# Optimization experiments

Measured on AMD Instinct MI355X. Metric: run time of the kernel, lower is better.

Reference implementation:

```python
import jax, jax.numpy as jnp
import numpy as np

N, E, G, D, L = 200000, 400000, 1024, 300, 5
BN_EPS = 1e-5


def setup_inputs() -> dict:
    key = jax.random.key(0)
    ks = jax.random.split(key, 14)
    s = 0.1  # param init scale
    return {
        "atomic_number": jax.random.randint(ks[0], (N,), 0, 120),
        "chirality_type": jax.random.randint(ks[1], (N,), 0, 3),
        "bond_type": jax.random.randint(ks[2], (E,), 0, 6),
        "bond_direction_type": jax.random.randint(ks[3], (E,), 0, 3),
        "src": jax.random.randint(ks[4], (E,), 0, N),
        "dst": jax.random.randint(ks[5], (E,), 0, N),
        "graph_ids": jnp.sort(jax.random.randint(ks[6], (N,), 0, G)),
        "num_graphs": G,
        "node_emb0": jax.random.normal(ks[7], (120, D), jnp.float32) * s,
        "node_emb1": jax.random.normal(ks[8], (3, D), jnp.float32) * s,
        "edge_emb0": jax.random.normal(ks[9], (L, 6, D), jnp.float32) * s,
        "edge_emb1": jax.random.normal(ks[10], (L, 3, D), jnp.float32) * s,
        "W1": jax.random.normal(ks[11], (L, D, 2 * D), jnp.float32) * (1.0 / np.sqrt(D)),
        "b1": jnp.zeros((L, 2 * D), jnp.float32),
        "W2": jax.random.normal(ks[12], (L, 2 * D, D), jnp.float32) * (1.0 / np.sqrt(2 * D)),
        "b2": jnp.zeros((L, D), jnp.float32),
        "bn_gamma": jnp.ones((L, D), jnp.float32),
        "bn_beta": jnp.zeros((L, D), jnp.float32),
        "bn_mean": jnp.zeros((L, D), jnp.float32),
        "bn_var": jnp.ones((L, D), jnp.float32),
        "Wd": jax.random.normal(ks[13], (D, 256), jnp.float32) * (1.0 / np.sqrt(D)),
        "bd": jnp.zeros((256,), jnp.float32),
    }


def reference(atomic_number, chirality_type, bond_type, bond_direction_type,
              src, dst, graph_ids, num_graphs,
              node_emb0, node_emb1, edge_emb0, edge_emb1,
              W1, b1, W2, b2, bn_gamma, bn_beta, bn_mean, bn_var, Wd, bd):
    n = atomic_number.shape[0]
    # input node embedding: sum of the two categorical lookups
    h = node_emb0[atomic_number] + node_emb1[chirality_type]  # [N, D]
    for l in range(L):
        # per-layer edge embedding (sum of bond-type / bond-direction lookups)
        e = edge_emb0[l][bond_type] + edge_emb1[l][bond_direction_type]  # [E, D]
        # message u_add_e, sum reduce onto destination nodes
        m = h[src] + e
        agg = jax.ops.segment_sum(m, dst, num_segments=n)  # [N, D]
        # GIN MLP: Linear(D,2D) -> ReLU -> Linear(2D,D)
        h = jax.nn.relu(agg @ W1[l] + b1[l]) @ W2[l] + b2[l]
        # BatchNorm1d in eval mode (running stats)
        h = (h - bn_mean[l]) * jax.lax.rsqrt(bn_var[l] + BN_EPS) * bn_gamma[l] + bn_beta[l]
        if l < L - 1:  # ReLU on all but last layer (dropout is identity in eval)
            h = jax.nn.relu(h)
    # AvgPooling over nodes of each graph
    gsum = jax.ops.segment_sum(h, graph_ids, num_segments=num_graphs)  # [G, D]
    cnt = jax.ops.segment_sum(jnp.ones((n, 1), h.dtype), graph_ids, num_segments=num_graphs)
    gavg = gsum / jnp.maximum(cnt, 1.0)
    # head: Dropout (eval identity) + Linear(300, 256), then squeeze (no-op here)
    return jnp.squeeze(gavg @ Wd + bd)
```

## Files before the change

### kernel.cpp

```cpp
#include <hip/hip_runtime.h>
#include <hip/hip_bf16.h>
#include <hip/hip_fp16.h>

#define D 300
#define D2 150
#define HD 600
#define NLAYERS 5
#define BN_EPS 1e-5f

#define KS1 10
#define NT1 5
#define KS2 20
#define NT2 3
#define P1 (NT1*KS1*4096)
#define P2 (NT2*KS2*4096)

#define SCAN_BLK 1024

typedef _Float16 f16x8 __attribute__((ext_vector_type(8)));
typedef __attribute__((ext_vector_type(4))) float f32x4;

__device__ inline ushort f2h(float x) {
    __half h = __float2half(x);
    return *reinterpret_cast<ushort*>(&h);
}
__device__ inline float h2f(ushort u) {
    __half h;
    *reinterpret_cast<ushort*>(&h) = u;
    return __half2float(h);
}
__device__ inline uint pack2h(float lo, float hi) {
    return (uint)f2h(lo) | ((uint)f2h(hi) << 16);
}

__global__ __launch_bounds__(256) void zero_kernel(uint4* __restrict__ p, long n4)
{
    long i = (long)blockIdx.x * blockDim.x + threadIdx.x;
    long stride = (long)gridDim.x * blockDim.x;
    uint4 z = make_uint4(0u, 0u, 0u, 0u);
    for (; i < n4; i += stride) p[i] = z;
}

__global__ __launch_bounds__(256) void embed_kernel(
    const int* __restrict__ an, const int* __restrict__ ch,
    const float* __restrict__ e0, const float* __restrict__ e1,
    uint* __restrict__ h_u, int N)
{
    int node = blockIdx.x * 4 + (threadIdx.x >> 6);
    if (node >= N) return;
    int lane = threadIdx.x & 63;
    const float* r0 = e0 + (size_t)an[node] * D;
    const float* r1 = e1 + (size_t)ch[node] * D;
    uint* hr = h_u + (size_t)node * D2;
    for (int d2 = lane; d2 < D2; d2 += 64) {
        float2 a = *(const float2*)(r0 + d2 * 2);
        float2 b = *(const float2*)(r1 + d2 * 2);
        hr[d2] = pack2h(a.x + b.x, a.y + b.y);
    }
}

__global__ __launch_bounds__(256) void count_kernel(
    const int* __restrict__ dst, int* __restrict__ deg, int E)
{
    int e = blockIdx.x * 256 + threadIdx.x;
    if (e < E) atomicAdd(&deg[dst[e]], 1);
}

__global__ __launch_bounds__(256) void scan_part_kernel(
    const int* __restrict__ deg, int* __restrict__ part, int N)
{
    __shared__ int sm[256];
    int b = blockIdx.x, t = threadIdx.x;
    int base = b * SCAN_BLK + t * 4;
    int s = 0;
#pragma unroll
    for (int j = 0; j < 4; ++j) { int i = base + j; if (i < N) s += deg[i]; }
    sm[t] = s;
    __syncthreads();
    for (int off = 128; off > 0; off >>= 1) {
        if (t < off) sm[t] += sm[t + off];
        __syncthreads();
    }
    if (t == 0) part[b] = sm[0];
}

__global__ __launch_bounds__(256) void scan_top_kernel(int* __restrict__ part, int NB)
{
    __shared__ int sm[256];
    int t = threadIdx.x;
    int own = (t < NB) ? part[t] : 0;
    sm[t] = own;
    __syncthreads();
    for (int off = 1; off < 256; off <<= 1) {
        int u = (t >= off) ? sm[t - off] : 0;
        __syncthreads();
        sm[t] += u;
        __syncthreads();
    }
    if (t < NB) part[t] = sm[t] - own;
}

__global__ __launch_bounds__(256) void scan_write_kernel(
    const int* __restrict__ deg, const int* __restrict__ part,
    int* __restrict__ offsets, int* __restrict__ cursor, int N, int E)
{
    __shared__ int sm[256];
    int b = blockIdx.x, t = threadIdx.x;
    int base = b * SCAN_BLK + t * 4;
    int v[4], s = 0;
#pragma unroll
    for (int j = 0; j < 4; ++j) { int i = base + j; v[j] = (i < N) ? deg[i] : 0; s += v[j]; }
    int own = s;
    sm[t] = s;
    __syncthreads();
    for (int off = 1; off < 256; off <<= 1) {
        int u = (t >= off) ? sm[t - off] : 0;
        __syncthreads();
        sm[t] += u;
        __syncthreads();
    }
    int ex = sm[t] - own + part[b];
#pragma unroll
    for (int j = 0; j < 4; ++j) {
        int i = base + j;
        if (i < N) { offsets[i] = ex; cursor[i] = ex; ex += v[j]; }
    }
    if (b == 0 && t == 0) offsets[N] = E;
}

__global__ __launch_bounds__(256) void scatter_kernel(
    const int* __restrict__ dst, int* __restrict__ cursor,
    int* __restrict__ csr, int E)
{
    int e = blockIdx.x * 256 + threadIdx.x;
    if (e < E) {
        int pos = atomicAdd(&cursor[dst[e]], 1);
        csr[pos] = e;
    }
}

__global__ __launch_bounds__(256) void eprep_kernel(
    const int* __restrict__ csr, const int* __restrict__ src,
    const int* __restrict__ bt, const int* __restrict__ bd,
    int* __restrict__ esrc, unsigned char* __restrict__ ecomb, int E)
{
    int p = blockIdx.x * 256 + threadIdx.x;
    if (p < E) {
        int e = csr[p];
        esrc[p] = src[e];
        ecomb[p] = (unsigned char)(bt[e] * 3 + bd[e]);
    }
}

__global__ __launch_bounds__(256) void etab_kernel(
    const float* __restrict__ ee0, const float* __restrict__ ee1,
    uint* __restrict__ etab)
{
    int i = blockIdx.x * 256 + threadIdx.x;
    const int total = NLAYERS * 18 * D2;
    if (i >= total) return;
    int d2 = i % D2;
    int rest = i / D2;
    int c = rest % 18, l = rest / 18;
    int btv = c / 3, bdv = c % 3;
    const float* r0 = ee0 + ((size_t)l * 6 + btv) * D + d2 * 2;
    const float* r1 = ee1 + ((size_t)l * 3 + bdv) * D + d2 * 2;
    etab[i] = pack2h(r0[0] + r1[0], r0[1] + r1[1]);
}

__global__ __launch_bounds__(256) void aggregate_kernel(
    const uint* __restrict__ h_u,
    const uint* __restrict__ etab_l,
    const int* __restrict__ esrc, const unsigned char* __restrict__ ecomb,
    const int* __restrict__ offsets,
    uint* __restrict__ agg_u, int N)
{
    int v = blockIdx.x * 4 + (threadIdx.x >> 6);
    if (v >= N) return;
    int lane = threadIdx.x & 63;
    int p0 = offsets[v], p1 = offsets[v + 1];
    float ax[3] = {0.f, 0.f, 0.f}, ay[3] = {0.f, 0.f, 0.f};
    for (int p = p0; p < p1; ++p) {
        int s = esrc[p];
        int c = ecomb[p];
        const uint* hr = h_u + (size_t)s * D2;
        const uint* er = etab_l + c * D2;
#pragma unroll
        for (int it = 0; it < 3; ++it) {
            int d2 = lane + it * 64;
            if (d2 < D2) {
                uint hv = hr[d2];
                uint ev = er[d2];
                ax[it] += h2f((ushort)(hv & 0xffffu)) + h2f((ushort)(ev & 0xffffu));
                ay[it] += h2f((ushort)(hv >> 16))     + h2f((ushort)(ev >> 16));
            }
        }
    }
    uint* ag = agg_u + (size_t)v * D2;
#pragma unroll
    for (int it = 0; it < 3; ++it) {
        int d2 = lane + it * 64;
        if (d2 < D2) ag[d2] = pack2h(ax[it], ay[it]);
    }
}

__global__ void prep_bn_kernel(
    const float* __restrict__ b2, const float* __restrict__ gamma,
    const float* __restrict__ beta, const float* __restrict__ mean,
    const float* __restrict__ var, float* __restrict__ scale2,
    float* __restrict__ shift2, int n)
{
    int i = blockIdx.x * blockDim.x + threadIdx.x;
    if (i >= n) return;
    float s = gamma[i] * rsqrtf(var[i] + BN_EPS);
    scale2[i] = s;
    shift2[i] = (b2[i] - mean[i]) * s + beta[i];
}

__global__ __launch_bounds__(256) void conv_w_kernel(
    const float* __restrict__ W1, const float* __restrict__ W2,
    ushort* __restrict__ w1h, ushort* __restrict__ w2h)
{
    int i = blockIdx.x * blockDim.x + threadIdx.x;
    const int PER = P1 + P2;
    if (i >= NLAYERS * PER) return;
    int l = i / PER;
    int r = i - l * PER;
    float v;
    ushort* ph;
    if (r < P1) {
        int pos = r;
        int j = pos & 7, c = (pos >> 3) & 127, kg = (pos >> 10) & 3;
        int rest = pos >> 12;
        int ks = rest % KS1, nt = rest / KS1;
        int k = ks * 32 + kg * 8 + j, n = nt * 128 + c;
        v = (k < D && n < HD) ? W1[(size_t)l * D * HD + (size_t)k * HD + n] : 0.f;
        ph = w1h + (size_t)l * P1 + pos;
    } else {
        int pos = r - P1;
        int j = pos & 7, c = (pos >> 3) & 127, kg = (pos >> 10) & 3;
        int rest = pos >> 12;
        int ks = rest % KS2, nt = rest / KS2;
        int k = ks * 32 + kg * 8 + j, n = nt * 128 + c;
        v = (k < HD && n < D) ? W2[(size_t)l * HD * D + (size_t)k * D + n] : 0.f;
        ph = w2h + (size_t)l * P2 + pos;
    }
    *ph = f2h(v);
}

template<bool RELU2>
__global__ __launch_bounds__(512, 4) void fused_mlp_kernel(
    const ushort* __restrict__ Ain,
    const uint4* __restrict__ B1,
    const uint4* __restrict__ B2,
    const float* __restrict__ bias1,
    const float* __restrict__ scale2,
    const float* __restrict__ shift2,
    ushort* __restrict__ Hout,
    int M)
{
    __shared__ ushort lds[KS2 * 4 * 64 * 8];
    ushort* ldsA = lds;
    ushort* ldsH = lds;

    int t = threadIdx.x;
    int lane = t & 63;
    int wid = t >> 6;
    int lanelo = lane & 15;
    int kg = lane >> 4;
    int m0 = blockIdx.x * 64;

    {
        const uint2* Ag = (const uint2*)Ain;
#pragma unroll
        for (int i = 0; i < 10; ++i) {
            int g = t + i * 512;
            int r = g / 80, c2 = g - r * 80;
            uint2 v = make_uint2(0u, 0u);
            if (c2 < 75 && (m0 + r) < M) v = Ag[(size_t)(m0 + r) * 75 + c2];
            int k0 = c2 * 4;
            int ks = k0 >> 5, g2 = (k0 >> 3) & 3, j = k0 & 7;
            ((uint2*)ldsA)[(((ks * 4 + g2) * 64 + r) * 8 + j) >> 2] = v;
        }
    }
    __syncthreads();

    {
        f32x4 acc[4][5];
#pragma unroll
        for (int mi = 0; mi < 4; ++mi)
#pragma unroll
            for (int ni = 0; ni < 5; ++ni) {
                f32x4 z = {0.f, 0.f, 0.f, 0.f};
                acc[mi][ni] = z;
            }

        int addrb[5];
#pragma unroll
        for (int ni = 0; ni < 5; ++ni) {
            int col = wid * 80 + ni * 16 + lanelo;
            int nt = col >> 7, c = col & 127;
            addrb[ni] = nt * (KS1 * 512) + kg * 128 + c;
        }

        uint4 bn[5];
#pragma unroll
        for (int ni = 0; ni < 5; ++ni) bn[ni] = B1[addrb[ni]];

        const f16x8* ap = (const f16x8*)ldsA;
#pragma unroll
        for (int ks = 0; ks < KS1; ++ks) {
            uint4 bc[5];
#pragma unroll
            for (int ni = 0; ni < 5; ++ni) bc[ni] = bn[ni];
            if (ks + 1 < KS1) {
#pragma unroll
                for (int ni = 0; ni < 5; ++ni) bn[ni] = B1[addrb[ni] + (ks + 1) * 512];
            }
            int ab = (ks * 4 + kg) * 64 + lanelo;
            f16x8 a0 = ap[ab];
            f16x8 a1 = ap[ab + 16];
            f16x8 a2 = ap[ab + 32];
            f16x8 a3 = ap[ab + 48];
#pragma unroll
            for (int ni = 0; ni < 5; ++ni) {
                f16x8 b = *(const f16x8*)&bc[ni];
                acc[0][ni] = __builtin_amdgcn_mfma_f32_16x16x32_f16(a0, b, acc[0][ni], 0, 0, 0);
                acc[1][ni] = __builtin_amdgcn_mfma_f32_16x16x32_f16(a1, b, acc[1][ni], 0, 0, 0);
                acc[2][ni] = __builtin_amdgcn_mfma_f32_16x16x32_f16(a2, b, acc[2][ni], 0, 0, 0);
                acc[3][ni] = __builtin_amdgcn_mfma_f32_16x16x32_f16(a3, b, acc[3][ni], 0, 0, 0);
            }
        }

        __syncthreads();

#pragma unroll
        for (int ni = 0; ni < 5; ++ni) {
            int col = wid * 80 + ni * 16 + lanelo;
            float bias = (col < HD) ? bias1[col] : 0.f;
            int ks2 = col >> 5, g2 = (col >> 3) & 3, j2 = col & 7;
            int base = ((ks2 * 4 + g2) * 64) * 8 + j2;
#pragma unroll
            for (int mi = 0; mi < 4; ++mi) {
                int r0 = mi * 16 + kg * 4;
#pragma unroll
                for (int r = 0; r < 4; ++r) {
                    float y = acc[mi][ni][r] + bias;
                    y = fmaxf(y, 0.f);
                    ldsH[base + (r0 + r) * 8] = f2h(y);
                }
            }
        }
    }
    __syncthreads();

    {
        f32x4 acc[4][3];
#pragma unroll
        for (int mi = 0; mi < 4; ++mi)
#pragma unroll
            for (int ni = 0; ni < 3; ++ni) {
                f32x4 z = {0.f, 0.f, 0.f, 0.f};
                acc[mi][ni] = z;
            }

        int addrb[3];
#pragma unroll
        for (int ni = 0; ni < 3; ++ni) {
            int col = wid * 48 + ni * 16 + lanelo;
            int nt = col >> 7, c = col & 127;
            addrb[ni] = nt * (KS2 * 512) + kg * 128 + c;
        }

        uint4 bn[3];
#pragma unroll
        for (int ni = 0; ni < 3; ++ni) bn[ni] = B2[addrb[ni]];

        const f16x8* hp = (const f16x8*)ldsH;
#pragma unroll
        for (int ks = 0; ks < KS2; ++ks) {
            uint4 bc[3];
#pragma unroll
            for (int ni = 0; ni < 3; ++ni) bc[ni] = bn[ni];
            if (ks + 1 < KS2) {
#pragma unroll
                for (int ni = 0; ni < 3; ++ni) bn[ni] = B2[addrb[ni] + (ks + 1) * 512];
            }
            int ab = (ks * 4 + kg) * 64 + lanelo;
            f16x8 a0 = hp[ab];
            f16x8 a1 = hp[ab + 16];
            f16x8 a2 = hp[ab + 32];
            f16x8 a3 = hp[ab + 48];
#pragma unroll
            for (int ni = 0; ni < 3; ++ni) {
                f16x8 b = *(const f16x8*)&bc[ni];
                acc[0][ni] = __builtin_amdgcn_mfma_f32_16x16x32_f16(a0, b, acc[0][ni], 0, 0, 0);
                acc[1][ni] = __builtin_amdgcn_mfma_f32_16x16x32_f16(a1, b, acc[1][ni], 0, 0, 0);
                acc[2][ni] = __builtin_amdgcn_mfma_f32_16x16x32_f16(a2, b, acc[2][ni], 0, 0, 0);
                acc[3][ni] = __builtin_amdgcn_mfma_f32_16x16x32_f16(a3, b, acc[3][ni], 0, 0, 0);
            }
        }

#pragma unroll
        for (int ni = 0; ni < 3; ++ni) {
            int col = wid * 48 + ni * 16 + lanelo;
            if (col < D) {
                float sc = scale2[col];
                float sh = shift2[col];
#pragma unroll
                for (int mi = 0; mi < 4; ++mi) {
                    int rbase = m0 + mi * 16 + kg * 4;
#pragma unroll
                    for (int r = 0; r < 4; ++r) {
                        int row = rbase + r;
                        if (row < M) {
                            float y = acc[mi][ni][r] * sc + sh;
                            if (RELU2) y = fmaxf(y, 0.f);
                            Hout[(size_t)row * D + col] = f2h(y);
                        }
                    }
                }
            }
        }
    }
}

__global__ __launch_bounds__(320) void pool_kernel(
    const ushort* __restrict__ h, const int* __restrict__ gid,
    float* __restrict__ gavg, int N)
{
    int g = blockIdx.x;
    int lo = 0, hi = N;
    while (lo < hi) { int mid = (lo + hi) >> 1; if (gid[mid] < g) lo = mid + 1; else hi = mid; }
    int start = lo;
    lo = start; hi = N;
    while (lo < hi) { int mid = (lo + hi) >> 1; if (gid[mid] <= g) lo = mid + 1; else hi = mid; }
    int end = lo;
    int d = threadIdx.x;
    if (d >= D) return;
    float s = 0.f;
    for (int i = start; i < end; ++i) s += h2f(h[(size_t)i * D + d]);
    float cnt = (float)(end - start);
    gavg[(size_t)g * D + d] = s / fmaxf(cnt, 1.f);
}

__global__ __launch_bounds__(256) void head_kernel(
    const float* __restrict__ gavg, const float* __restrict__ Wd,
    const float* __restrict__ bd, float* __restrict__ out)
{
    int g = blockIdx.x;
    int j = threadIdx.x;
    float s = bd[j];
    const float* gr = gavg + (size_t)g * D;
    for (int d = 0; d < D; ++d) s = fmaf(gr[d], Wd[(size_t)d * 256 + j], s);
    out[(size_t)g * 256 + j] = s;
}

extern "C" void kernel_launch(void* const* d_in, const int* in_sizes, int n_in,
                              void* d_out, int out_size, void* d_ws, size_t ws_size,
                              hipStream_t stream)
{
    const int*   atomic_number = (const int*)d_in[0];
    const int*   chirality     = (const int*)d_in[1];
    const int*   bond_type     = (const int*)d_in[2];
    const int*   bond_dir      = (const int*)d_in[3];
    const int*   src           = (const int*)d_in[4];
    const int*   dst           = (const int*)d_in[5];
    const int*   graph_ids     = (const int*)d_in[6];
    const float* node_emb0     = (const float*)d_in[8];
    const float* node_emb1     = (const float*)d_in[9];
    const float* edge_emb0     = (const float*)d_in[10];
    const float* edge_emb1     = (const float*)d_in[11];
    const float* W1            = (const float*)d_in[12];
    const float* b1            = (const float*)d_in[13];
    const float* W2            = (const float*)d_in[14];
    const float* b2            = (const float*)d_in[15];
    const float* bn_gamma      = (const float*)d_in[16];
    const float* bn_beta       = (const float*)d_in[17];
    const float* bn_mean       = (const float*)d_in[18];
    const float* bn_var        = (const float*)d_in[19];
    const float* Wd            = (const float*)d_in[20];
    const float* bd            = (const float*)d_in[21];

    int N = in_sizes[0];
    int E = in_sizes[2];
    int G = out_size / 256;
    float* out = (float*)d_out;

    char* ws = (char*)d_ws;
    size_t offs = 0;
    auto take = [&](size_t nbytes) -> char* {
        char* p = ws + offs;
        offs += (nbytes + 255) & ~(size_t)255;
        return p;
    };
    ushort* w1h    = (ushort*)take((size_t)NLAYERS * P1 * 2);
    ushort* w2h    = (ushort*)take((size_t)NLAYERS * P2 * 2);
    ushort* h      = (ushort*)take((size_t)N * D * 2);
    ushort* agg    = (ushort*)take((size_t)N * D * 2);
    int*    deg    = (int*)take((size_t)N * 4);
    int*    offsets= (int*)take((size_t)(N + 1) * 4);
    int*    cursor = (int*)take((size_t)N * 4);
    int*    csr    = (int*)take((size_t)E * 4);
    int*    esrc   = (int*)take((size_t)E * 4);
    unsigned char* ecomb = (unsigned char*)take((size_t)E);
    uint*   etab   = (uint*)take((size_t)NLAYERS * 18 * D2 * 4);
    int*    part   = (int*)take((size_t)256 * 4);
    float*  gavg   = (float*)take((size_t)G * D * 4);
    float*  scale2 = (float*)take((size_t)NLAYERS * D * 4);
    float*  shift2 = (float*)take((size_t)NLAYERS * D * 4);

    prep_bn_kernel<<<(NLAYERS * D + 255) / 256, 256, 0, stream>>>(
        b2, bn_gamma, bn_beta, bn_mean, bn_var, scale2, shift2, NLAYERS * D);
    {
        int T = NLAYERS * (P1 + P2);
        conv_w_kernel<<<(T + 255) / 256, 256, 0, stream>>>(W1, W2, w1h, w2h);
    }
    etab_kernel<<<(NLAYERS * 18 * D2 + 255) / 256, 256, 0, stream>>>(
        edge_emb0, edge_emb1, etab);
    embed_kernel<<<(N + 3) / 4, 256, 0, stream>>>(
        atomic_number, chirality, node_emb0, node_emb1, (uint*)h, N);

    int NB = (N + SCAN_BLK - 1) / SCAN_BLK;
    zero_kernel<<<(int)(((size_t)N + 1023) / 1024), 256, 0, stream>>>((uint4*)deg, (long)N / 4);
    count_kernel<<<(E + 255) / 256, 256, 0, stream>>>(dst, deg, E);
    scan_part_kernel<<<NB, 256, 0, stream>>>(deg, part, N);
    scan_top_kernel<<<1, 256, 0, stream>>>(part, NB);
    scan_write_kernel<<<NB, 256, 0, stream>>>(deg, part, offsets, cursor, N, E);
    scatter_kernel<<<(E + 255) / 256, 256, 0, stream>>>(dst, cursor, csr, E);
    eprep_kernel<<<(E + 255) / 256, 256, 0, stream>>>(csr, src, bond_type, bond_dir, esrc, ecomb, E);

    int mlp_grid = (N + 63) / 64;
    for (int l = 0; l < NLAYERS; ++l) {
        aggregate_kernel<<<(N + 3) / 4, 256, 0, stream>>>(
            (const uint*)h,
            etab + (size_t)l * 18 * D2,
            esrc, ecomb, offsets, (uint*)agg, N);

        if (l < NLAYERS - 1)
            fused_mlp_kernel<true><<<mlp_grid, 512, 0, stream>>>(
                agg,
                (const uint4*)(w1h + (size_t)l * P1),
                (const uint4*)(w2h + (size_t)l * P2),
                b1 + (size_t)l * HD,
                scale2 + (size_t)l * D, shift2 + (size_t)l * D,
                h, N);
        else
            fused_mlp_kernel<false><<<mlp_grid, 512, 0, stream>>>(
                agg,
                (const uint4*)(w1h + (size_t)l * P1),
                (const uint4*)(w2h + (size_t)l * P2),
                b1 + (size_t)l * HD,
                scale2 + (size_t)l * D, shift2 + (size_t)l * D,
                h, N);
    }

    pool_kernel<<<G, 320, 0, stream>>>(h, graph_ids, gavg, N);
    head_kernel<<<G, 256, 0, stream>>>(gavg, Wd, bd, out);
}
```

Before: 1.997 ms.

## Fuse neighbor aggregation into MLP kernel with ping-pong node buffers

Drops the separate aggregate kernel. Each MLP block now gathers its 64 destination rows' messages directly into swizzled LDS, so the agg array is never written to or read back from global memory. It also adds an XOR swizzle on the A-tile LDS layout, packs half pairs via shuffles for the hidden tile, and stages the output tile in LDS for coalesced row stores. Ping-pong h buffers avoid read/write hazards across layers. The cost is that the irregular gather now runs inside a heavy 512-thread MFMA kernel: each wave handles 8 rows serially, which may lower latency hiding and adds load imbalance.

```diff
diff --git a/kernel.cpp b/kernel.cpp
--- a/kernel.cpp
+++ b/kernel.cpp
@@ -166,42 +166,6 @@
     const float* r0 = ee0 + ((size_t)l * 6 + btv) * D + d2 * 2;
     const float* r1 = ee1 + ((size_t)l * 3 + bdv) * D + d2 * 2;
     etab[i] = pack2h(r0[0] + r1[0], r0[1] + r1[1]);
-}
-
-__global__ __launch_bounds__(256) void aggregate_kernel(
-    const uint* __restrict__ h_u,
-    const uint* __restrict__ etab_l,
-    const int* __restrict__ esrc, const unsigned char* __restrict__ ecomb,
-    const int* __restrict__ offsets,
-    uint* __restrict__ agg_u, int N)
-{
-    int v = blockIdx.x * 4 + (threadIdx.x >> 6);
-    if (v >= N) return;
-    int lane = threadIdx.x & 63;
-    int p0 = offsets[v], p1 = offsets[v + 1];
-    float ax[3] = {0.f, 0.f, 0.f}, ay[3] = {0.f, 0.f, 0.f};
-    for (int p = p0; p < p1; ++p) {
-        int s = esrc[p];
-        int c = ecomb[p];
-        const uint* hr = h_u + (size_t)s * D2;
-        const uint* er = etab_l + c * D2;
-#pragma unroll
-        for (int it = 0; it < 3; ++it) {
-            int d2 = lane + it * 64;
-            if (d2 < D2) {
-                uint hv = hr[d2];
-                uint ev = er[d2];
-                ax[it] += h2f((ushort)(hv & 0xffffu)) + h2f((ushort)(ev & 0xffffu));
-                ay[it] += h2f((ushort)(hv >> 16))     + h2f((ushort)(ev >> 16));
-            }
-        }
-    }
-    uint* ag = agg_u + (size_t)v * D2;
-#pragma unroll
-    for (int it = 0; it < 3; ++it) {
-        int d2 = lane + it * 64;
-        if (d2 < D2) ag[d2] = pack2h(ax[it], ay[it]);
-    }
 }
 
 __global__ void prep_bn_kernel(
@@ -250,18 +214,19 @@
 
 template<bool RELU2>
 __global__ __launch_bounds__(512, 4) void fused_mlp_kernel(
-    const ushort* __restrict__ Ain,
+    const uint* __restrict__ Hin,
+    const uint* __restrict__ etab_l,
+    const int* __restrict__ esrc, const unsigned char* __restrict__ ecomb,
+    const int* __restrict__ offsets,
     const uint4* __restrict__ B1,
     const uint4* __restrict__ B2,
     const float* __restrict__ bias1,
     const float* __restrict__ scale2,
     const float* __restrict__ shift2,
-    ushort* __restrict__ Hout,
+    uint* __restrict__ Hout,
     int M)
 {
     __shared__ ushort lds[KS2 * 4 * 64 * 8];
-    ushort* ldsA = lds;
-    ushort* ldsH = lds;
 
     int t = threadIdx.x;
     int lane = t & 63;
@@ -271,16 +236,46 @@
     int m0 = blockIdx.x * 64;
 
     {
-        const uint2* Ag = (const uint2*)Ain;
-#pragma unroll
-        for (int i = 0; i < 10; ++i) {
-            int g = t + i * 512;
-            int r = g / 80, c2 = g - r * 80;
-            uint2 v = make_uint2(0u, 0u);
-            if (c2 < 75 && (m0 + r) < M) v = Ag[(size_t)(m0 + r) * 75 + c2];
-            int k0 = c2 * 4;
-            int ks = k0 >> 5, g2 = (k0 >> 3) & 3, j = k0 & 7;
-            ((uint2*)ldsA)[(((ks * 4 + g2) * 64 + r) * 8 + j) >> 2] = v;
+        uint* ldsAu = (uint*)lds;
+        int rbase = wid * 8;
+        for (int rr = 0; rr < 8; ++rr) {
+            int rowl = rbase + rr;
+            int v = m0 + rowl;
+            float ax0 = 0.f, ay0 = 0.f, ax1 = 0.f, ay1 = 0.f, ax2 = 0.f, ay2 = 0.f;
+            if (v < M) {
+                int p0 = offsets[v], p1 = offsets[v + 1];
+                for (int p = p0; p < p1; ++p) {
+                    int s = esrc[p];
+                    int c = ecomb[p];
+                    const uint* hr = Hin + (size_t)s * D2;
+                    const uint* er = etab_l + c * D2;
+                    int d0 = lane, d1 = lane + 64, dq = lane + 128;
+                    uint hv0 = hr[d0], ev0 = er[d0];
+                    uint hv1 = hr[d1], ev1 = er[d1];
+                    uint hv2 = 0u, ev2 = 0u;
+                    if (dq < D2) { hv2 = hr[dq]; ev2 = er[dq]; }
+                    ax0 += h2f((ushort)(hv0 & 0xffffu)) + h2f((ushort)(ev0 & 0xffffu));
+                    ay0 += h2f((ushort)(hv0 >> 16))     + h2f((ushort)(ev0 >> 16));
+                    ax1 += h2f((ushort)(hv1 & 0xffffu)) + h2f((ushort)(ev1 & 0xffffu));
+                    ay1 += h2f((ushort)(hv1 >> 16))     + h2f((ushort)(ev1 >> 16));
+                    ax2 += h2f((ushort)(hv2 & 0xffffu)) + h2f((ushort)(ev2 & 0xffffu));
+                    ay2 += h2f((ushort)(hv2 >> 16))     + h2f((ushort)(ev2 >> 16));
+                }
+            }
+            {
+                int d2 = lane;
+                int q = d2 >> 2;
+                ldsAu[(q * 64 + (rowl ^ (q & 7))) * 4 + (d2 & 3)] = pack2h(ax0, ay0);
+                d2 = lane + 64;
+                q = d2 >> 2;
+                ldsAu[(q * 64 + (rowl ^ (q & 7))) * 4 + (d2 & 3)] = pack2h(ax1, ay1);
+                d2 = lane + 128;
+                if (d2 < 160) {
+                    uint val = (d2 < D2) ? pack2h(ax2, ay2) : 0u;
+                    q = d2 >> 2;
+                    ldsAu[(q * 64 + (rowl ^ (q & 7))) * 4 + (d2 & 3)] = val;
+                }
+            }
         }
     }
     __syncthreads();
@@ -307,7 +302,7 @@
 #pragma unroll
         for (int ni = 0; ni < 5; ++ni) bn[ni] = B1[addrb[ni]];
 
-        const f16x8* ap = (const f16x8*)ldsA;
+        const f16x8* ap = (const f16x8*)lds;
 #pragma unroll
         for (int ks = 0; ks < KS1; ++ks) {
             uint4 bc[5];
@@ -317,7 +312,8 @@
 #pragma unroll
                 for (int ni = 0; ni < 5; ++ni) bn[ni] = B1[addrb[ni] + (ks + 1) * 512];
             }
-            int ab = (ks * 4 + kg) * 64 + lanelo;
+            int q1 = ks * 4 + kg;
+            int ab = q1 * 64 + (lanelo ^ (q1 & 7));
             f16x8 a0 = ap[ab];
             f16x8 a1 = ap[ab + 16];
             f16x8 a2 = ap[ab + 32];
@@ -334,20 +330,22 @@
 
         __syncthreads();
 
+        uint* ldsHu = (uint*)lds;
 #pragma unroll
         for (int ni = 0; ni < 5; ++ni) {
             int col = wid * 80 + ni * 16 + lanelo;
             float bias = (col < HD) ? bias1[col] : 0.f;
             int ks2 = col >> 5, g2 = (col >> 3) & 3, j2 = col & 7;
-            int base = ((ks2 * 4 + g2) * 64) * 8 + j2;
+            int dbase = (ks2 * 4 + g2) * 256 + (j2 >> 1);
 #pragma unroll
             for (int mi = 0; mi < 4; ++mi) {
                 int r0 = mi * 16 + kg * 4;
 #pragma unroll
                 for (int r = 0; r < 4; ++r) {
-                    float y = acc[mi][ni][r] + bias;
-                    y = fmaxf(y, 0.f);
-                    ldsH[base + (r0 + r) * 8] = f2h(y);
+                    float y = fmaxf(acc[mi][ni][r] + bias, 0.f);
+                    float yn = __shfl_xor(y, 1);
+                    if ((lanelo & 1) == 0)
+                        ldsHu[dbase + (r0 + r) * 4] = pack2h(y, yn);
                 }
             }
         }
@@ -376,7 +374,7 @@
 #pragma unroll
         for (int ni = 0; ni < 3; ++ni) bn[ni] = B2[addrb[ni]];
 
-        const f16x8* hp = (const f16x8*)ldsH;
+        const f16x8* hp = (const f16x8*)lds;
 #pragma unroll
         for (int ks = 0; ks < KS2; ++ks) {
             uint4 bc[3];
@@ -401,25 +399,39 @@
             }
         }
 
+        __syncthreads();
+
+        uint* stg = (uint*)lds;
 #pragma unroll
         for (int ni = 0; ni < 3; ++ni) {
             int col = wid * 48 + ni * 16 + lanelo;
-            if (col < D) {
-                float sc = scale2[col];
-                float sh = shift2[col];
-#pragma unroll
-                for (int mi = 0; mi < 4; ++mi) {
-                    int rbase = m0 + mi * 16 + kg * 4;
-#pragma unroll
-                    for (int r = 0; r < 4; ++r) {
-                        int row = rbase + r;
-                        if (row < M) {
-                            float y = acc[mi][ni][r] * sc + sh;
-                            if (RELU2) y = fmaxf(y, 0.f);
-                            Hout[(size_t)row * D + col] = f2h(y);
-                        }
-                    }
+            float sc = 1.f, sh = 0.f;
+            if (col < D) { sc = scale2[col]; sh = shift2[col]; }
+#pragma unroll
+            for (int mi = 0; mi < 4; ++mi) {
+                int r0 = mi * 16 + kg * 4;
+#pragma unroll
+                for (int r = 0; r < 4; ++r) {
+                    float y = acc[mi][ni][r] * sc + sh;
+                    if (RELU2) y = fmaxf(y, 0.f);
+                    float yn = __shfl_xor(y, 1);
+                    if ((lanelo & 1) == 0 && col < D)
+                        stg[(r0 + r) * 154 + (col >> 1)] = pack2h(y, yn);
                 }
+            }
+        }
+    }
+    __syncthreads();
+
+    {
+        const uint* stg = (const uint*)lds;
+#pragma unroll
+        for (int i = 0; i < 19; ++i) {
+            int g = t + i * 512;
+            if (g < 64 * 150) {
+                int row = g / 150, c = g - row * 150;
+                if (m0 + row < M)
+                    Hout[(size_t)(m0 + row) * D2 + c] = stg[row * 154 + c];
             }
         }
     }
@@ -496,8 +508,8 @@
     };
     ushort* w1h    = (ushort*)take((size_t)NLAYERS * P1 * 2);
     ushort* w2h    = (ushort*)take((size_t)NLAYERS * P2 * 2);
-    ushort* h      = (ushort*)take((size_t)N * D * 2);
-    ushort* agg    = (ushort*)take((size_t)N * D * 2);
+    uint*   h0     = (uint*)take((size_t)N * D2 * 4);
+    uint*   h1     = (uint*)take((size_t)N * D2 * 4);
     int*    deg    = (int*)take((size_t)N * 4);
     int*    offsets= (int*)take((size_t)(N + 1) * 4);
     int*    cursor = (int*)take((size_t)N * 4);
@@ -519,7 +531,7 @@
     etab_kernel<<<(NLAYERS * 18 * D2 + 255) / 256, 256, 0, stream>>>(
         edge_emb0, edge_emb1, etab);
     embed_kernel<<<(N + 3) / 4, 256, 0, stream>>>(
-        atomic_number, chirality, node_emb0, node_emb1, (uint*)h, N);
+        atomic_number, chirality, node_emb0, node_emb1, h0, N);
 
     int NB = (N + SCAN_BLK - 1) / SCAN_BLK;
     zero_kernel<<<(int)(((size_t)N + 1023) / 1024), 256, 0, stream>>>((uint4*)deg, (long)N / 4);
@@ -532,29 +544,26 @@
 
     int mlp_grid = (N + 63) / 64;
     for (int l = 0; l < NLAYERS; ++l) {
-        aggregate_kernel<<<(N + 3) / 4, 256, 0, stream>>>(
-            (const uint*)h,
-            etab + (size_t)l * 18 * D2,
-            esrc, ecomb, offsets, (uint*)agg, N);
-
+        const uint* hin = (l & 1) ? h1 : h0;
+        uint* hout      = (l & 1) ? h0 : h1;
         if (l < NLAYERS - 1)
             fused_mlp_kernel<true><<<mlp_grid, 512, 0, stream>>>(
-                agg,
+                hin, etab + (size_t)l * 18 * D2, esrc, ecomb, offsets,
                 (const uint4*)(w1h + (size_t)l * P1),
                 (const uint4*)(w2h + (size_t)l * P2),
                 b1 + (size_t)l * HD,
                 scale2 + (size_t)l * D, shift2 + (size_t)l * D,
-                h, N);
+                hout, N);
         else
             fused_mlp_kernel<false><<<mlp_grid, 512, 0, stream>>>(
-                agg,
+                hin, etab + (size_t)l * 18 * D2, esrc, ecomb, offsets,
                 (const uint4*)(w1h + (size_t)l * P1),
                 (const uint4*)(w2h + (size_t)l * P2),
                 b1 + (size_t)l * HD,
                 scale2 + (size_t)l * D, shift2 + (size_t)l * D,
-                h, N);
-    }
-
-    pool_kernel<<<G, 320, 0, stream>>>(h, graph_ids, gavg, N);
+                hout, N);
+    }
+
+    pool_kernel<<<G, 320, 0, stream>>>((const ushort*)h1, graph_ids, gavg, N);
     head_kernel<<<G, 256, 0, stream>>>(gavg, Wd, bd, out);
 }
```

Measured after the change: 1.841 ms. -7.8%, faster.
